# Performance work log

Measured on AMD Instinct MI355X. Metric: run time of the kernel, lower is better.

## Reference

```python
import jax, jax.numpy as jnp
import numpy as np

VOCAB = 4000
U = 30000   # unique tokens
M = 12      # max mid-char length
H = 256     # hidden_size
O = 768     # output_size
B = 16      # sequences
L = 2048    # tokens per sequence (equal lengths -> jit-friendly reassemble)


def setup_inputs() -> dict:
    key = jax.random.key(0)
    ks = jax.random.split(key, 8)
    emb_table = jax.random.normal(ks[0], (VOCAB, H), dtype=jnp.float32)
    emb_table = emb_table.at[0].set(0.0)  # padding_idx=0
    head_w = jax.random.normal(ks[1], (3 * H, O), dtype=jnp.float32) * 0.02
    head_b = jax.random.normal(ks[2], (O,), dtype=jnp.float32) * 0.02
    first = jax.random.randint(ks[3], (U,), 0, VOCAB, dtype=jnp.int32)
    mid = jax.random.randint(ks[4], (U, M), 0, VOCAB, dtype=jnp.int32)
    last = jax.random.randint(ks[5], (U,), 0, VOCAB, dtype=jnp.int32)
    inv_i = jax.random.randint(ks[6], (B * L,), 0, U, dtype=jnp.int32)
    return {"emb_table": emb_table, "head_w": head_w, "head_b": head_b,
            "first": first, "mid": mid, "last": last, "inv_i": inv_i,
            "batch": B, "seq_len": L}


def reference(emb_table, head_w, head_b, first, mid, last, inv_i, batch, seq_len):
    def lookup(ids):
        # emulate padding_idx=0: id 0 contributes a zero vector
        v = emb_table[ids]
        return v * (ids != 0)[..., None].astype(v.dtype)

    rep = jnp.concatenate(
        [lookup(first), lookup(mid).sum(axis=1), lookup(last)], axis=-1)  # [U, 3H]
    out = rep @ head_w + head_b                                           # [U, O]
    tok = out[inv_i].reshape(batch, seq_len, -1)                          # [B, L, O]
    # reassemble: one zero row before and after each sequence (F.pad (1,1) on time)
    return jnp.pad(tok, ((0, 0), (1, 1), (0, 0)))                         # [B, L+2, O]
```

## Files before the change

### kernel.cpp

```cpp
#include <hip/hip_runtime.h>

#define VOCAB 4000
#define UNIQ 30000
#define MIDN 12
#define HID 256
#define OUT 768
#define BATCH 16
#define SEQ 2048

#define NXCD 8
#define XCOLS 96
#define SUBC 16
#define TCHUNK 2048
#define NCHUNK 16
#define TPASS 256
#define NPASS 8
#define PLANE 32008

typedef __attribute__((ext_vector_type(8))) short short8;
typedef __attribute__((ext_vector_type(4))) float f32x4;
typedef __attribute__((ext_vector_type(4))) unsigned int u32x4;
typedef __attribute__((ext_vector_type(2))) unsigned int u32x2;

__device__ __forceinline__ float bitsf(unsigned int x) {
    float f; __builtin_memcpy(&f, &x, 4); return f;
}
__device__ __forceinline__ unsigned short f2bf(float f) {
    unsigned int x;
    __builtin_memcpy(&x, &f, 4);
    x += 0x7fff + ((x >> 16) & 1);
    return (unsigned short)(x >> 16);
}

__global__ __launch_bounds__(256) void build_idsT(
    const int* __restrict__ first, const int* __restrict__ mid,
    const int* __restrict__ last, const int* __restrict__ inv_i,
    short* __restrict__ idsT)
{
    int t = blockIdx.x * 256 + threadIdx.x;
    if (t >= BATCH * SEQ) return;
    int u = inv_i[t];
    int4 m0 = *reinterpret_cast<const int4*>(&mid[u * MIDN]);
    int4 m1 = *reinterpret_cast<const int4*>(&mid[u * MIDN + 4]);
    int4 m2 = *reinterpret_cast<const int4*>(&mid[u * MIDN + 8]);
    short ids[16];
    ids[0]  = (short)first[u];
    ids[1]  = (short)m0.x; ids[2]  = (short)m0.y; ids[3]  = (short)m0.z; ids[4]  = (short)m0.w;
    ids[5]  = (short)m1.x; ids[6]  = (short)m1.y; ids[7]  = (short)m1.z; ids[8]  = (short)m1.w;
    ids[9]  = (short)m2.x; ids[10] = (short)m2.y; ids[11] = (short)m2.z; ids[12] = (short)m2.w;
    ids[13] = (short)last[u];
    ids[14] = 0; ids[15] = 0;
    *reinterpret_cast<short8*>(&idsT[(size_t)t * 16])     = *reinterpret_cast<short8*>(&ids[0]);
    *reinterpret_cast<short8*>(&idsT[(size_t)t * 16 + 8]) = *reinterpret_cast<short8*>(&ids[8]);
}

__global__ __launch_bounds__(256) void conv_w(
    const float* __restrict__ W, unsigned short* __restrict__ Wt)
{
    __shared__ float T[32][33];
    const int s  = blockIdx.z;
    const int n0 = blockIdx.x * 32;
    const int h0 = blockIdx.y * 32;
    const int tx = threadIdx.x & 31;
    const int ty = threadIdx.x >> 5;

    #pragma unroll
    for (int k = 0; k < 4; ++k) {
        int h = ty + 8 * k;
        T[h][tx] = W[(size_t)(s * HID + h0 + h) * OUT + n0 + tx];
    }
    __syncthreads();
    #pragma unroll
    for (int k = 0; k < 4; ++k) {
        int n = ty + 8 * k;
        Wt[(size_t)(s * OUT + n0 + n) * HID + h0 + tx] = f2bf(T[tx][n]);
    }
}

__global__ __launch_bounds__(256) void proj_mfma(
    const float* __restrict__ E,
    const unsigned short* __restrict__ Wt,
    unsigned short* __restrict__ P,
    unsigned short* __restrict__ Pmid)
{
    const int s  = blockIdx.z;
    const int n0 = blockIdx.x * 128;
    const int m0 = blockIdx.y * 128;
    const unsigned short* Wts = Wt + (size_t)s * OUT * HID;

    __shared__ short As[128][40];
    __shared__ short Bs[128][40];

    const int tid  = threadIdx.x;
    const int lane = tid & 63;
    const int w    = tid >> 6;
    const int wm   = w >> 1;
    const int wn   = w & 1;
    const int lo   = lane & 15;
    const int hi   = lane >> 4;

    f32x4 acc[4][4] = {};

    for (int kt = 0; kt < HID; kt += 32) {
        #pragma unroll
        for (int p = 0; p < 2; ++p) {
            int idx = p * 256 + tid;
            int row = idx >> 2;
            int ko  = (idx & 3) * 8;
            int gm  = m0 + row;
            f32x4 e0 = {}, e1 = {};
            if (gm < VOCAB) {
                e0 = *reinterpret_cast<const f32x4*>(&E[(size_t)gm * HID + kt + ko]);
                e1 = *reinterpret_cast<const f32x4*>(&E[(size_t)gm * HID + kt + ko + 4]);
            }
            short8 v;
            v[0] = (short)f2bf(e0.x); v[1] = (short)f2bf(e0.y);
            v[2] = (short)f2bf(e0.z); v[3] = (short)f2bf(e0.w);
            v[4] = (short)f2bf(e1.x); v[5] = (short)f2bf(e1.y);
            v[6] = (short)f2bf(e1.z); v[7] = (short)f2bf(e1.w);
            *reinterpret_cast<short8*>(&As[row][ko]) = v;
        }
        #pragma unroll
        for (int p = 0; p < 2; ++p) {
            int idx = p * 256 + tid;
            int col = idx >> 2;
            int ko  = (idx & 3) * 8;
            short8 v = *reinterpret_cast<const short8*>(
                &Wts[(size_t)(n0 + col) * HID + kt + ko]);
            *reinterpret_cast<short8*>(&Bs[col][ko]) = v;
        }
        __syncthreads();

        short8 a[4], b[4];
        #pragma unroll
        for (int f = 0; f < 4; ++f)
            a[f] = *reinterpret_cast<short8*>(&As[wm * 64 + f * 16 + lo][hi * 8]);
        #pragma unroll
        for (int f = 0; f < 4; ++f)
            b[f] = *reinterpret_cast<short8*>(&Bs[wn * 64 + f * 16 + lo][hi * 8]);
        #pragma unroll
        for (int fm = 0; fm < 4; ++fm)
            #pragma unroll
            for (int fn = 0; fn < 4; ++fn)
                acc[fm][fn] = __builtin_amdgcn_mfma_f32_16x16x32_bf16(
                    a[fm], b[fn], acc[fm][fn], 0, 0, 0);
        __syncthreads();
    }

    #pragma unroll
    for (int fm = 0; fm < 4; ++fm) {
        #pragma unroll
        for (int fn = 0; fn < 4; ++fn) {
            #pragma unroll
            for (int r = 0; r < 4; ++r) {
                int gm = m0 + wm * 64 + fm * 16 + hi * 4 + r;
                int gn = n0 + wn * 64 + fn * 16 + lo;
                if (gm < VOCAB) {
                    unsigned short val = f2bf(acc[fm][fn][r]);
                    if (s == 1) {
                        Pmid[((size_t)(gn >> 4) * VOCAB + gm) * SUBC + (gn & 15)] = val;
                    } else {
                        int so = (s == 0) ? 0 : 1;
                        unsigned int sl = (unsigned int)gn / XCOLS;
                        unsigned int cc = (unsigned int)gn - sl * XCOLS;
                        P[(((size_t)sl * 2 + so) * VOCAB + gm) * XCOLS + cc] = val;
                    }
                }
            }
        }
    }
}

extern __shared__ char lds_raw[];

__global__ __launch_bounds__(1024) void token_lds(
    const unsigned short* __restrict__ P,
    const unsigned short* __restrict__ Pmid,
    const short* __restrict__ idsT,
    const float* __restrict__ bias,
    float* __restrict__ out)
{
    const int xcd = blockIdx.x & 7;
    const int bi  = blockIdx.x >> 3;

    const int tid = threadIdx.x;
    const int l4  = tid & 3;
    const int grp = tid >> 2;

    char* myplane = lds_raw + l4 * PLANE;
    const unsigned short* Pbase = P + (size_t)xcd * 2 * VOCAB * XCOLS;

    int cur_sl = -1;

    #pragma unroll 1
    for (int k = 0; k < 3; ++k) {
        const int task = bi * 3 + k;
        const int sl   = task >> 4;
        const int ch   = task & 15;

        if (sl != cur_sl) {
            if (cur_sl >= 0) __syncthreads();
            const int sub = xcd * 6 + sl;
            const unsigned short* src = Pmid + (size_t)sub * VOCAB * SUBC;
            #pragma unroll
            for (int i = 0; i < 16; ++i) {
                int idx = i * 1024 + tid;
                if (idx < VOCAB * 4) {
                    int row = idx >> 2;
                    int q   = idx & 3;
                    uint2 v = *reinterpret_cast<const uint2*>(&src[row * SUBC + q * 4]);
                    *reinterpret_cast<uint2*>(lds_raw + q * PLANE + row * 8) = v;
                }
            }
            __syncthreads();
            cur_sl = sl;
        }

        const int csub = sl * SUBC + l4 * 4;
        const int colc = xcd * XCOLS + csub;
        const unsigned short* P0 = Pbase + csub;
        const unsigned short* P2 = Pbase + (size_t)VOCAB * XCOLS + csub;
        const f32x4 bv = *reinterpret_cast<const f32x4*>(&bias[colc]);

        const int t0 = ch * TCHUNK + grp;

#define LDIDS(lo_, hi_, tt_) { \
        const u32x4* _r = reinterpret_cast<const u32x4*>(&idsT[(size_t)(tt_) * 16]); \
        lo_ = _r[0]; hi_ = _r[1]; }

#define GATHER(fv_, lv_, lo_, hi_) { \
        int _fid = (int)((lo_).x & 0xffffu); \
        int _lid = (int)((hi_).z >> 16); \
        fv_ = *reinterpret_cast<const uint2*>(&P0[(size_t)_fid * XCOLS]); \
        lv_ = *reinterpret_cast<const uint2*>(&P2[(size_t)_lid * XCOLS]); }

        u32x4 ilA, ihA, ilB, ihB;
        uint2 fvA, lvA, fvB, lvB;

        LDIDS(ilA, ihA, t0);
        LDIDS(ilB, ihB, t0 + TPASS);
        GATHER(fvA, lvA, ilA, ihA);

        #pragma unroll
        for (int p = 0; p < NPASS; ++p) {
            const bool even = (p & 1) == 0;
            u32x4 clo = even ? ilA : ilB;
            u32x4 chi = even ? ihA : ihB;
            uint2 cfv = even ? fvA : fvB;
            uint2 clv = even ? lvA : lvB;

            if (p + 1 < NPASS) {
                if (even) { GATHER(fvB, lvB, ilB, ihB); }
                else      { GATHER(fvA, lvA, ilA, ihA); }
            }
            if (p + 2 < NPASS) {
                if (even) { LDIDS(ilA, ihA, t0 + (p + 2) * TPASS); }
                else      { LDIDS(ilB, ihB, t0 + (p + 2) * TPASS); }
            }

            int rid[MIDN];
            rid[0]  = (int)(clo.x >> 16);
            rid[1]  = (int)(clo.y & 0xffffu);
            rid[2]  = (int)(clo.y >> 16);
            rid[3]  = (int)(clo.z & 0xffffu);
            rid[4]  = (int)(clo.z >> 16);
            rid[5]  = (int)(clo.w & 0xffffu);
            rid[6]  = (int)(clo.w >> 16);
            rid[7]  = (int)(chi.x & 0xffffu);
            rid[8]  = (int)(chi.x >> 16);
            rid[9]  = (int)(chi.y & 0xffffu);
            rid[10] = (int)(chi.y >> 16);
            rid[11] = (int)(chi.z & 0xffffu);

            uint2 mv[MIDN];
            #pragma unroll
            for (int m = 0; m < MIDN; ++m)
                mv[m] = *reinterpret_cast<const uint2*>(myplane + rid[m] * 8);

            float a0 = bv.x, a1 = bv.y, a2 = bv.z, a3 = bv.w;
            #pragma unroll
            for (int m = 0; m < MIDN; ++m) {
                a0 += bitsf(mv[m].x << 16);
                a1 += bitsf(mv[m].x & 0xffff0000u);
                a2 += bitsf(mv[m].y << 16);
                a3 += bitsf(mv[m].y & 0xffff0000u);
            }
            a0 += bitsf(cfv.x << 16); a1 += bitsf(cfv.x & 0xffff0000u);
            a2 += bitsf(cfv.y << 16); a3 += bitsf(cfv.y & 0xffff0000u);
            a0 += bitsf(clv.x << 16); a1 += bitsf(clv.x & 0xffff0000u);
            a2 += bitsf(clv.y << 16); a3 += bitsf(clv.y & 0xffff0000u);

            const int t = t0 + p * TPASS;
            const int b = t >> 11;
            const int l = t & (SEQ - 1);
            float* dst = &out[((size_t)(b * (SEQ + 2) + l + 1)) * OUT + colc];
            f32x4 o = {a0, a1, a2, a3};
            __builtin_nontemporal_store(o, reinterpret_cast<f32x4*>(dst));
        }
#undef LDIDS
#undef GATHER
    }
}

__global__ void zero_pads(float* __restrict__ out)
{
    int j = blockIdx.x * blockDim.x + threadIdx.x;
    const int n4 = OUT / 4;
    if (j >= BATCH * 2 * n4) return;
    int b  = j / (2 * n4);
    int r  = (j / n4) & 1;
    int c4 = j % n4;
    int row = r ? (SEQ + 1) : 0;
    f32x4 z = {};
    *reinterpret_cast<f32x4*>(
        &out[((size_t)(b * (SEQ + 2) + row)) * OUT + c4 * 4]) = z;
}

extern "C" void kernel_launch(void* const* d_in, const int* in_sizes, int n_in,
                              void* d_out, int out_size, void* d_ws, size_t ws_size,
                              hipStream_t stream)
{
    const float* emb    = (const float*)d_in[0];
    const float* head_w = (const float*)d_in[1];
    const float* head_b = (const float*)d_in[2];
    const int*   first  = (const int*)d_in[3];
    const int*   mid    = (const int*)d_in[4];
    const int*   last   = (const int*)d_in[5];
    const int*   inv_i  = (const int*)d_in[6];
    float* out = (float*)d_out;

    char* ws = (char*)d_ws;
    unsigned short* P    = (unsigned short*)ws;
    unsigned short* Wt   = (unsigned short*)(ws + 12288000);
    unsigned short* Pmid = (unsigned short*)(ws + 13467648);
    short*          idsT = (short*)(ws + 19611648);

    build_idsT<<<(BATCH * SEQ + 255) / 256, 256, 0, stream>>>(
        first, mid, last, inv_i, idsT);

    dim3 gw(OUT / 32, HID / 32, 3);
    conv_w<<<gw, 256, 0, stream>>>(head_w, Wt);

    dim3 g1(OUT / 128, (VOCAB + 127) / 128, 3);
    proj_mfma<<<g1, 256, 0, stream>>>(emb, Wt, P, Pmid);

    token_lds<<<256, 1024, 4 * PLANE, stream>>>(P, Pmid, idsT, head_b, out);

    const int pad4 = BATCH * 2 * (OUT / 4);
    zero_pads<<<(pad4 + 255) / 256, 256, 0, stream>>>(out);
}
```

Baseline: 67.11 us.

## Merge prep kernels, fold pad zeroing, transpose projection, widen token gather

Merges the id-transpose and weight-convert kernels into one prep launch and folds the pad-row zeroing into the token kernel, which removes two launches. The projection GEMM swaps operand roles so each lane writes four contiguous bf16 outputs as one vector store instead of scattered scalar stores. The token kernel now gives each thread 8 columns via two LDS planes of 16-byte rows instead of 4 columns via four planes. This halves the number of index loads and passes per column but raises register pressure per thread.

```diff
diff --git a/kernel.cpp b/kernel.cpp
--- a/kernel.cpp
+++ b/kernel.cpp
@@ -13,14 +13,14 @@
 #define SUBC 16
 #define TCHUNK 2048
 #define NCHUNK 16
-#define TPASS 256
-#define NPASS 8
-#define PLANE 32008
+#define TPASS 512
+#define NPASS 4
+#define PLANE2 64016
 
 typedef __attribute__((ext_vector_type(8))) short short8;
 typedef __attribute__((ext_vector_type(4))) float f32x4;
 typedef __attribute__((ext_vector_type(4))) unsigned int u32x4;
-typedef __attribute__((ext_vector_type(2))) unsigned int u32x2;
+typedef __attribute__((ext_vector_type(4))) unsigned short u16x4;
 
 __device__ __forceinline__ float bitsf(unsigned int x) {
     float f; __builtin_memcpy(&f, &x, 4); return f;
@@ -32,48 +32,47 @@
     return (unsigned short)(x >> 16);
 }
 
-__global__ __launch_bounds__(256) void build_idsT(
+__global__ __launch_bounds__(256) void prep(
+    const float* __restrict__ W, unsigned short* __restrict__ Wt,
     const int* __restrict__ first, const int* __restrict__ mid,
     const int* __restrict__ last, const int* __restrict__ inv_i,
     short* __restrict__ idsT)
 {
-    int t = blockIdx.x * 256 + threadIdx.x;
-    if (t >= BATCH * SEQ) return;
-    int u = inv_i[t];
-    int4 m0 = *reinterpret_cast<const int4*>(&mid[u * MIDN]);
-    int4 m1 = *reinterpret_cast<const int4*>(&mid[u * MIDN + 4]);
-    int4 m2 = *reinterpret_cast<const int4*>(&mid[u * MIDN + 8]);
-    short ids[16];
-    ids[0]  = (short)first[u];
-    ids[1]  = (short)m0.x; ids[2]  = (short)m0.y; ids[3]  = (short)m0.z; ids[4]  = (short)m0.w;
-    ids[5]  = (short)m1.x; ids[6]  = (short)m1.y; ids[7]  = (short)m1.z; ids[8]  = (short)m1.w;
-    ids[9]  = (short)m2.x; ids[10] = (short)m2.y; ids[11] = (short)m2.z; ids[12] = (short)m2.w;
-    ids[13] = (short)last[u];
-    ids[14] = 0; ids[15] = 0;
-    *reinterpret_cast<short8*>(&idsT[(size_t)t * 16])     = *reinterpret_cast<short8*>(&ids[0]);
-    *reinterpret_cast<short8*>(&idsT[(size_t)t * 16 + 8]) = *reinterpret_cast<short8*>(&ids[8]);
-}
-
-__global__ __launch_bounds__(256) void conv_w(
-    const float* __restrict__ W, unsigned short* __restrict__ Wt)
-{
     __shared__ float T[32][33];
-    const int s  = blockIdx.z;
-    const int n0 = blockIdx.x * 32;
-    const int h0 = blockIdx.y * 32;
-    const int tx = threadIdx.x & 31;
-    const int ty = threadIdx.x >> 5;
-
-    #pragma unroll
-    for (int k = 0; k < 4; ++k) {
-        int h = ty + 8 * k;
-        T[h][tx] = W[(size_t)(s * HID + h0 + h) * OUT + n0 + tx];
-    }
-    __syncthreads();
-    #pragma unroll
-    for (int k = 0; k < 4; ++k) {
-        int n = ty + 8 * k;
-        Wt[(size_t)(s * OUT + n0 + n) * HID + h0 + tx] = f2bf(T[tx][n]);
+    if (blockIdx.z < 3) {
+        const int s  = blockIdx.z;
+        const int n0 = blockIdx.x * 32;
+        const int h0 = blockIdx.y * 32;
+        const int tx = threadIdx.x & 31;
+        const int ty = threadIdx.x >> 5;
+        #pragma unroll
+        for (int k = 0; k < 4; ++k) {
+            int h = ty + 8 * k;
+            T[h][tx] = W[(size_t)(s * HID + h0 + h) * OUT + n0 + tx];
+        }
+        __syncthreads();
+        #pragma unroll
+        for (int k = 0; k < 4; ++k) {
+            int n = ty + 8 * k;
+            Wt[(size_t)(s * OUT + n0 + n) * HID + h0 + tx] = f2bf(T[tx][n]);
+        }
+    } else {
+        int bid2 = blockIdx.y * 24 + blockIdx.x;
+        int t = bid2 * 256 + threadIdx.x;
+        if (t >= BATCH * SEQ) return;
+        int u = inv_i[t];
+        int4 m0 = *reinterpret_cast<const int4*>(&mid[u * MIDN]);
+        int4 m1 = *reinterpret_cast<const int4*>(&mid[u * MIDN + 4]);
+        int4 m2 = *reinterpret_cast<const int4*>(&mid[u * MIDN + 8]);
+        short ids[16];
+        ids[0]  = (short)first[u];
+        ids[1]  = (short)m0.x; ids[2]  = (short)m0.y; ids[3]  = (short)m0.z; ids[4]  = (short)m0.w;
+        ids[5]  = (short)m1.x; ids[6]  = (short)m1.y; ids[7]  = (short)m1.z; ids[8]  = (short)m1.w;
+        ids[9]  = (short)m2.x; ids[10] = (short)m2.y; ids[11] = (short)m2.z; ids[12] = (short)m2.w;
+        ids[13] = (short)last[u];
+        ids[14] = 0; ids[15] = 0;
+        *reinterpret_cast<short8*>(&idsT[(size_t)t * 16])     = *reinterpret_cast<short8*>(&ids[0]);
+        *reinterpret_cast<short8*>(&idsT[(size_t)t * 16 + 8]) = *reinterpret_cast<short8*>(&ids[8]);
     }
 }
 
@@ -83,9 +82,9 @@
     unsigned short* __restrict__ P,
     unsigned short* __restrict__ Pmid)
 {
-    const int s  = blockIdx.z;
-    const int n0 = blockIdx.x * 128;
-    const int m0 = blockIdx.y * 128;
+    const int s     = blockIdx.z;
+    const int vbase = blockIdx.x * 128;
+    const int cbase = blockIdx.y * 128;
     const unsigned short* Wts = Wt + (size_t)s * OUT * HID;
 
     __shared__ short As[128][40];
@@ -107,27 +106,27 @@
             int idx = p * 256 + tid;
             int row = idx >> 2;
             int ko  = (idx & 3) * 8;
-            int gm  = m0 + row;
+            short8 v = *reinterpret_cast<const short8*>(
+                &Wts[(size_t)(cbase + row) * HID + kt + ko]);
+            *reinterpret_cast<short8*>(&As[row][ko]) = v;
+        }
+        #pragma unroll
+        for (int p = 0; p < 2; ++p) {
+            int idx = p * 256 + tid;
+            int row = idx >> 2;
+            int ko  = (idx & 3) * 8;
+            int gv  = vbase + row;
             f32x4 e0 = {}, e1 = {};
-            if (gm < VOCAB) {
-                e0 = *reinterpret_cast<const f32x4*>(&E[(size_t)gm * HID + kt + ko]);
-                e1 = *reinterpret_cast<const f32x4*>(&E[(size_t)gm * HID + kt + ko + 4]);
+            if (gv < VOCAB) {
+                e0 = *reinterpret_cast<const f32x4*>(&E[(size_t)gv * HID + kt + ko]);
+                e1 = *reinterpret_cast<const f32x4*>(&E[(size_t)gv * HID + kt + ko + 4]);
             }
             short8 v;
             v[0] = (short)f2bf(e0.x); v[1] = (short)f2bf(e0.y);
             v[2] = (short)f2bf(e0.z); v[3] = (short)f2bf(e0.w);
             v[4] = (short)f2bf(e1.x); v[5] = (short)f2bf(e1.y);
             v[6] = (short)f2bf(e1.z); v[7] = (short)f2bf(e1.w);
-            *reinterpret_cast<short8*>(&As[row][ko]) = v;
-        }
-        #pragma unroll
-        for (int p = 0; p < 2; ++p) {
-            int idx = p * 256 + tid;
-            int col = idx >> 2;
-            int ko  = (idx & 3) * 8;
-            short8 v = *reinterpret_cast<const short8*>(
-                &Wts[(size_t)(n0 + col) * HID + kt + ko]);
-            *reinterpret_cast<short8*>(&Bs[col][ko]) = v;
+            *reinterpret_cast<short8*>(&Bs[row][ko]) = v;
         }
         __syncthreads();
 
@@ -151,20 +150,23 @@
     for (int fm = 0; fm < 4; ++fm) {
         #pragma unroll
         for (int fn = 0; fn < 4; ++fn) {
-            #pragma unroll
-            for (int r = 0; r < 4; ++r) {
-                int gm = m0 + wm * 64 + fm * 16 + hi * 4 + r;
-                int gn = n0 + wn * 64 + fn * 16 + lo;
-                if (gm < VOCAB) {
-                    unsigned short val = f2bf(acc[fm][fn][r]);
-                    if (s == 1) {
-                        Pmid[((size_t)(gn >> 4) * VOCAB + gm) * SUBC + (gn & 15)] = val;
-                    } else {
-                        int so = (s == 0) ? 0 : 1;
-                        unsigned int sl = (unsigned int)gn / XCOLS;
-                        unsigned int cc = (unsigned int)gn - sl * XCOLS;
-                        P[(((size_t)sl * 2 + so) * VOCAB + gm) * XCOLS + cc] = val;
-                    }
+            const int c0 = cbase + wm * 64 + fm * 16 + hi * 4;
+            const int v  = vbase + wn * 64 + fn * 16 + lo;
+            if (v < VOCAB) {
+                u16x4 vals;
+                vals.x = f2bf(acc[fm][fn][0]);
+                vals.y = f2bf(acc[fm][fn][1]);
+                vals.z = f2bf(acc[fm][fn][2]);
+                vals.w = f2bf(acc[fm][fn][3]);
+                if (s == 1) {
+                    *reinterpret_cast<u16x4*>(
+                        &Pmid[((size_t)(c0 >> 4) * VOCAB + v) * SUBC + (c0 & 15)]) = vals;
+                } else {
+                    const int so = (s == 0) ? 0 : 1;
+                    const unsigned int sl = (unsigned int)c0 / XCOLS;
+                    const unsigned int cc = (unsigned int)c0 - sl * XCOLS;
+                    *reinterpret_cast<u16x4*>(
+                        &P[(((size_t)sl * 2 + so) * VOCAB + v) * XCOLS + cc]) = vals;
                 }
             }
         }
@@ -184,11 +186,21 @@
     const int bi  = blockIdx.x >> 3;
 
     const int tid = threadIdx.x;
-    const int l4  = tid & 3;
-    const int grp = tid >> 2;
-
-    char* myplane = lds_raw + l4 * PLANE;
+    const int l2  = tid & 1;
+    const int grp = tid >> 1;
+
+    char* myplane = lds_raw + l2 * PLANE2;
     const unsigned short* Pbase = P + (size_t)xcd * 2 * VOCAB * XCOLS;
+
+    if (bi == 0 && tid < 768) {
+        int r  = tid / 24;
+        int c4 = tid % 24;
+        int b  = r >> 1;
+        int row = (r & 1) ? (b * (SEQ + 2) + SEQ + 1) : (b * (SEQ + 2));
+        f32x4 z = {};
+        *reinterpret_cast<f32x4*>(
+            &out[(size_t)row * OUT + xcd * XCOLS + c4 * 4]) = z;
+    }
 
     int cur_sl = -1;
 
@@ -203,24 +215,25 @@
             const int sub = xcd * 6 + sl;
             const unsigned short* src = Pmid + (size_t)sub * VOCAB * SUBC;
             #pragma unroll
-            for (int i = 0; i < 16; ++i) {
+            for (int i = 0; i < 8; ++i) {
                 int idx = i * 1024 + tid;
-                if (idx < VOCAB * 4) {
-                    int row = idx >> 2;
-                    int q   = idx & 3;
-                    uint2 v = *reinterpret_cast<const uint2*>(&src[row * SUBC + q * 4]);
-                    *reinterpret_cast<uint2*>(lds_raw + q * PLANE + row * 8) = v;
+                if (idx < VOCAB * 2) {
+                    int row  = idx >> 1;
+                    int half = idx & 1;
+                    u32x4 v = *reinterpret_cast<const u32x4*>(&src[row * SUBC + half * 8]);
+                    *reinterpret_cast<u32x4*>(lds_raw + half * PLANE2 + row * 16) = v;
                 }
             }
             __syncthreads();
             cur_sl = sl;
         }
 
-        const int csub = sl * SUBC + l4 * 4;
+        const int csub = sl * SUBC + l2 * 8;
         const int colc = xcd * XCOLS + csub;
         const unsigned short* P0 = Pbase + csub;
         const unsigned short* P2 = Pbase + (size_t)VOCAB * XCOLS + csub;
-        const f32x4 bv = *reinterpret_cast<const f32x4*>(&bias[colc]);
+        const f32x4 bv0 = *reinterpret_cast<const f32x4*>(&bias[colc]);
+        const f32x4 bv1 = *reinterpret_cast<const f32x4*>(&bias[colc + 4]);
 
         const int t0 = ch * TCHUNK + grp;
 
@@ -231,11 +244,11 @@
 #define GATHER(fv_, lv_, lo_, hi_) { \
         int _fid = (int)((lo_).x & 0xffffu); \
         int _lid = (int)((hi_).z >> 16); \
-        fv_ = *reinterpret_cast<const uint2*>(&P0[(size_t)_fid * XCOLS]); \
-        lv_ = *reinterpret_cast<const uint2*>(&P2[(size_t)_lid * XCOLS]); }
+        fv_ = *reinterpret_cast<const u32x4*>(&P0[(size_t)_fid * XCOLS]); \
+        lv_ = *reinterpret_cast<const u32x4*>(&P2[(size_t)_lid * XCOLS]); }
 
         u32x4 ilA, ihA, ilB, ihB;
-        uint2 fvA, lvA, fvB, lvB;
+        u32x4 fvA, lvA, fvB, lvB;
 
         LDIDS(ilA, ihA, t0);
         LDIDS(ilB, ihB, t0 + TPASS);
@@ -246,8 +259,8 @@
             const bool even = (p & 1) == 0;
             u32x4 clo = even ? ilA : ilB;
             u32x4 chi = even ? ihA : ihB;
-            uint2 cfv = even ? fvA : fvB;
-            uint2 clv = even ? lvA : lvB;
+            u32x4 cfv = even ? fvA : fvB;
+            u32x4 clv = even ? lvA : lvB;
 
             if (p + 1 < NPASS) {
                 if (even) { GATHER(fvB, lvB, ilB, ihB); }
@@ -272,48 +285,41 @@
             rid[10] = (int)(chi.y >> 16);
             rid[11] = (int)(chi.z & 0xffffu);
 
-            uint2 mv[MIDN];
+            u32x4 mv[MIDN];
             #pragma unroll
             for (int m = 0; m < MIDN; ++m)
-                mv[m] = *reinterpret_cast<const uint2*>(myplane + rid[m] * 8);
-
-            float a0 = bv.x, a1 = bv.y, a2 = bv.z, a3 = bv.w;
+                mv[m] = *reinterpret_cast<const u32x4*>(myplane + rid[m] * 16);
+
+            float a0 = bv0.x, a1 = bv0.y, a2 = bv0.z, a3 = bv0.w;
+            float a4 = bv1.x, a5 = bv1.y, a6 = bv1.z, a7 = bv1.w;
             #pragma unroll
             for (int m = 0; m < MIDN; ++m) {
-                a0 += bitsf(mv[m].x << 16);
-                a1 += bitsf(mv[m].x & 0xffff0000u);
-                a2 += bitsf(mv[m].y << 16);
-                a3 += bitsf(mv[m].y & 0xffff0000u);
+                a0 += bitsf(mv[m].x << 16); a1 += bitsf(mv[m].x & 0xffff0000u);
+                a2 += bitsf(mv[m].y << 16); a3 += bitsf(mv[m].y & 0xffff0000u);
+                a4 += bitsf(mv[m].z << 16); a5 += bitsf(mv[m].z & 0xffff0000u);
+                a6 += bitsf(mv[m].w << 16); a7 += bitsf(mv[m].w & 0xffff0000u);
             }
             a0 += bitsf(cfv.x << 16); a1 += bitsf(cfv.x & 0xffff0000u);
             a2 += bitsf(cfv.y << 16); a3 += bitsf(cfv.y & 0xffff0000u);
+            a4 += bitsf(cfv.z << 16); a5 += bitsf(cfv.z & 0xffff0000u);
+            a6 += bitsf(cfv.w << 16); a7 += bitsf(cfv.w & 0xffff0000u);
             a0 += bitsf(clv.x << 16); a1 += bitsf(clv.x & 0xffff0000u);
             a2 += bitsf(clv.y << 16); a3 += bitsf(clv.y & 0xffff0000u);
+            a4 += bitsf(clv.z << 16); a5 += bitsf(clv.z & 0xffff0000u);
+            a6 += bitsf(clv.w << 16); a7 += bitsf(clv.w & 0xffff0000u);
 
             const int t = t0 + p * TPASS;
             const int b = t >> 11;
             const int l = t & (SEQ - 1);
             float* dst = &out[((size_t)(b * (SEQ + 2) + l + 1)) * OUT + colc];
-            f32x4 o = {a0, a1, a2, a3};
-            __builtin_nontemporal_store(o, reinterpret_cast<f32x4*>(dst));
+            f32x4 o0 = {a0, a1, a2, a3};
+            f32x4 o1 = {a4, a5, a6, a7};
+            __builtin_nontemporal_store(o0, reinterpret_cast<f32x4*>(dst));
+            __builtin_nontemporal_store(o1, reinterpret_cast<f32x4*>(dst + 4));
         }
 #undef LDIDS
 #undef GATHER
     }
-}
-
-__global__ void zero_pads(float* __restrict__ out)
-{
-    int j = blockIdx.x * blockDim.x + threadIdx.x;
-    const int n4 = OUT / 4;
-    if (j >= BATCH * 2 * n4) return;
-    int b  = j / (2 * n4);
-    int r  = (j / n4) & 1;
-    int c4 = j % n4;
-    int row = r ? (SEQ + 1) : 0;
-    f32x4 z = {};
-    *reinterpret_cast<f32x4*>(
-        &out[((size_t)(b * (SEQ + 2) + row)) * OUT + c4 * 4]) = z;
 }
 
 extern "C" void kernel_launch(void* const* d_in, const int* in_sizes, int n_in,
@@ -335,17 +341,11 @@
     unsigned short* Pmid = (unsigned short*)(ws + 13467648);
     short*          idsT = (short*)(ws + 19611648);
 
-    build_idsT<<<(BATCH * SEQ + 255) / 256, 256, 0, stream>>>(
-        first, mid, last, inv_i, idsT);
-
-    dim3 gw(OUT / 32, HID / 32, 3);
-    conv_w<<<gw, 256, 0, stream>>>(head_w, Wt);
-
-    dim3 g1(OUT / 128, (VOCAB + 127) / 128, 3);
+    dim3 gp(24, 8, 4);
+    prep<<<gp, 256, 0, stream>>>(head_w, Wt, first, mid, last, inv_i, idsT);
+
+    dim3 g1(32, 6, 3);
     proj_mfma<<<g1, 256, 0, stream>>>(emb, Wt, P, Pmid);
 
-    token_lds<<<256, 1024, 4 * PLANE, stream>>>(P, Pmid, idsT, head_b, out);
-
-    const int pad4 = BATCH * 2 * (OUT / 4);
-    zero_pads<<<(pad4 + 255) / 256, 256, 0, stream>>>(out);
-}
+    token_lds<<<256, 1024, 2 * PLANE2, stream>>>(P, Pmid, idsT, head_b, out);
+}
```

Result: slower. 87.16 us (+29.9%).
